# Kernel tuning notes

Hardware: AMD Instinct MI355X
Metric: run time of the kernel (lower is better)

Reference implementation:

```python
import jax, jax.numpy as jnp
import numpy as np

B, S, D, H, DF, L, V, MAXLEN = 8, 1024, 768, 12, 3072, 6, 32000, 2048
HD = D // H
EPS = 1e-5

def _pe(max_length, d_model):
    position = jnp.arange(max_length, dtype=jnp.float32)[:, None]
    i = jnp.arange(d_model, dtype=jnp.float32)[None, :]
    angles = position * (1.0 / jnp.power(10000.0, 2.0 * jnp.floor(i / 2.0) / d_model))
    pe = jnp.zeros((max_length, d_model), dtype=jnp.float32)
    pe = pe.at[:, 0::2].set(jnp.sin(angles[:, 0::2]))
    pe = pe.at[:, 1::2].set(jnp.cos(angles[:, 1::2]))
    return pe

def _layernorm(x, g, b):
    mu = jnp.mean(x, axis=-1, keepdims=True)
    var = jnp.mean((x - mu) ** 2, axis=-1, keepdims=True)
    return (x - mu) * jax.lax.rsqrt(var + EPS) * g + b

def setup_inputs() -> dict:
    key = jax.random.key(0)
    ks = jax.random.split(key, 16)
    s = 0.02
    emb = jax.random.normal(ks[0], (V, D), jnp.float32) * s
    emb = emb.at[0].set(0.0)  # padding_idx=0
    inp = {
        'input_ids': jax.random.randint(ks[1], (B, S), 0, V),
        'emb': emb,
        'pe': _pe(MAXLEN, D),
        'Wq': jax.random.normal(ks[2], (L, D, D), jnp.float32) * s,
        'bq': jnp.zeros((L, D), jnp.float32),
        'Wk': jax.random.normal(ks[3], (L, D, D), jnp.float32) * s,
        'bk': jnp.zeros((L, D), jnp.float32),
        'Wv': jax.random.normal(ks[4], (L, D, D), jnp.float32) * s,
        'bv': jnp.zeros((L, D), jnp.float32),
        'W1': jax.random.normal(ks[5], (L, DF, D), jnp.float32) * s,
        'b1': jnp.zeros((L, DF), jnp.float32),
        'W2': jax.random.normal(ks[6], (L, D, DF), jnp.float32) * s,
        'b2': jnp.zeros((L, D), jnp.float32),
        'ln1_g': jnp.ones((L, D), jnp.float32),
        'ln1_b': jnp.zeros((L, D), jnp.float32),
        'ln2_g': jnp.ones((L, D), jnp.float32),
        'ln2_b': jnp.zeros((L, D), jnp.float32),
    }
    return inp

def _mha(x, Wq, bq, Wk, bk, Wv, bv):
    b, s, _ = x.shape
    q = (x @ Wq.T + bq).reshape(b, H, s, HD)  # faithful to torch .view (no transpose)
    k = (x @ Wk.T + bk).reshape(b, H, s, HD)
    v = (x @ Wv.T + bv).reshape(b, H, s, HD)
    scores = jnp.einsum('bhqd,bhkd->bhqk', q, k) / (HD ** 0.5)
    att = jax.nn.softmax(scores, axis=-1)
    o = jnp.einsum('bhqk,bhkd->bhqd', att, v)
    return o.transpose(0, 2, 1, 3).reshape(b, s, D)

def reference(input_ids, emb, pe, Wq, bq, Wk, bk, Wv, bv, W1, b1, W2, b2, ln1_g, ln1_b, ln2_g, ln2_b):
    x = emb[input_ids] + pe[:input_ids.shape[1], :]
    # dropout is identity in eval mode
    for l in range(L):
        h1 = _mha(x, Wq[l], bq[l], Wk[l], bk[l], Wv[l], bv[l])
        y1 = _layernorm(x + h1, ln1_g[l], ln1_b[l])
        h2 = jax.nn.relu(y1 @ W1[l].T + b1[l]) @ W2[l].T + b2[l]
        x = _layernorm(y1 + h2, ln2_g[l], ln2_b[l])
    return x
```

## Files before the change

kernel.cpp:

```cpp
#include <hip/hip_runtime.h>


typedef _Float16 f16;
typedef _Float16 half4 __attribute__((ext_vector_type(4)));
typedef _Float16 half8 __attribute__((ext_vector_type(8)));
typedef float f32x4 __attribute__((ext_vector_type(4)));
typedef float f32x16 __attribute__((ext_vector_type(16)));

constexpr int Bn = 8, Sn = 1024, Dn = 768, Hn = 12, HDn = 64, DFn = 3072, Ln = 6;
constexpr int BS = Bn * Sn;

__device__ __forceinline__ void glds16(const f16* g, f16* l) {
  __builtin_amdgcn_global_load_lds(
      (const __attribute__((address_space(1))) unsigned int*)g,
      (__attribute__((address_space(3))) unsigned int*)l, 16, 0, 0);
}

__device__ __forceinline__ float ex2(float x) {
#if __has_builtin(__builtin_amdgcn_exp2f)
  return __builtin_amdgcn_exp2f(x);
#else
  return exp2f(x);
#endif
}

__global__ __launch_bounds__(256) void pack_qkv(
    const float* __restrict__ Wq, const float* __restrict__ Wk, const float* __restrict__ Wv,
    const float* __restrict__ bq, const float* __restrict__ bk, const float* __restrict__ bv,
    f16* __restrict__ Wo, float* __restrict__ bo) {
  const long per = (long)Dn * Dn;
  const long t = (long)blockIdx.x * 256 + threadIdx.x;
  const long totalW4 = (long)Ln * 3 * per / 4;
  if (t < totalW4) {
    const long i = t * 4;
    const int l = (int)(i / (3 * per));
    long rem = i - (long)l * 3 * per;
    const int which = (int)(rem / per);
    const long e = rem - (long)which * per;
    const float* s = (which == 0) ? Wq : ((which == 1) ? Wk : Wv);
    const float4 v = *(const float4*)&s[(long)l * per + e];
    half4 h = {(f16)v.x, (f16)v.y, (f16)v.z, (f16)v.w};
    *(half4*)&Wo[i] = h;
  }
  if (t < (long)Ln * 3 * Dn) {
    int l = (int)(t / (3 * Dn));
    int rem = (int)(t % (3 * Dn));
    int which = rem / Dn, c = rem % Dn;
    const float* s = (which == 0) ? bq : ((which == 1) ? bk : bv);
    bo[t] = s[l * Dn + c];
  }
}

__global__ __launch_bounds__(256) void f32_to_f16_k(
    const float* __restrict__ src, f16* __restrict__ dst, long n) {
  long i = ((long)blockIdx.x * 256 + threadIdx.x) * 4;
  if (i < n) {
    float4 v = *(const float4*)&src[i];
    half4 h = {(f16)v.x, (f16)v.y, (f16)v.z, (f16)v.w};
    *(half4*)&dst[i] = h;
  }
}

__global__ __launch_bounds__(256) void embed_k(
    const int* __restrict__ ids, const float* __restrict__ emb, const float* __restrict__ pe,
    float* __restrict__ Xf, f16* __restrict__ Xh) {
  const int row = blockIdx.x;
  const int s = row & (Sn - 1);
  const int id = ids[row];
  const size_t eb = (size_t)id * Dn, pb = (size_t)s * Dn, ob = (size_t)row * Dn;
  for (int c = threadIdx.x; c < Dn; c += 256) {
    float v = emb[eb + c] + pe[pb + c];
    Xf[ob + c] = v;
    Xh[ob + c] = (f16)v;
  }
}

template <int MODE>
__global__ __launch_bounds__(256) void gemm_bt(
    const f16* __restrict__ A, const f16* __restrict__ Bw, const float* __restrict__ bias,
    float* __restrict__ outF, f16* __restrict__ o0, f16* __restrict__ o1, f16* __restrict__ o2,
    int M, int N, int K, int lda) {
  const int m0 = blockIdx.x * 128;
  const int n0 = blockIdx.y * 128;
  const int tid = threadIdx.x;
  const int lane = tid & 63, wave = tid >> 6;
  const int wm = wave & 1, wn = wave >> 1;
  const int l15 = lane & 15, l4 = lane >> 4;

  __shared__ __align__(16) f16 As[128 * 32];
  __shared__ __align__(16) f16 Bs[128 * 32];

  const f32x4 z4 = {0.f, 0.f, 0.f, 0.f};
  f32x4 acc[4][4];
#pragma unroll
  for (int i = 0; i < 4; i++)
#pragma unroll
    for (int j = 0; j < 4; j++) acc[i][j] = z4;

  const int sRow = wave * 32 + (lane >> 2);
  const int sCol = (lane & 3) * 8;
  const int kz = (MODE == 4) ? ((int)blockIdx.z * K) : 0;
  const f16* gA = A + (size_t)(m0 + sRow) * lda + kz + sCol;
  const f16* gB = Bw + (size_t)(n0 + sRow) * lda + kz + sCol;
  f16* lA0 = &As[(wave * 32) * 32];
  f16* lA1 = &As[(wave * 32 + 16) * 32];
  f16* lB0 = &Bs[(wave * 32) * 32];
  f16* lB1 = &Bs[(wave * 32 + 16) * 32];
  const size_t rowStep = (size_t)16 * lda;

  const int kr = 8 * l4;
  for (int k0 = 0; k0 < K; k0 += 32) {
    glds16(gA + k0, lA0);
    glds16(gA + k0 + rowStep, lA1);
    glds16(gB + k0, lB0);
    glds16(gB + k0 + rowStep, lB1);
    __syncthreads();
    half8 af[4], bfr[4];
#pragma unroll
    for (int i = 0; i < 4; i++) af[i] = *(const half8*)&As[(wm * 64 + i * 16 + l15) * 32 + kr];
#pragma unroll
    for (int j = 0; j < 4; j++) bfr[j] = *(const half8*)&Bs[(wn * 64 + j * 16 + l15) * 32 + kr];
#pragma unroll
    for (int i = 0; i < 4; i++)
#pragma unroll
      for (int j = 0; j < 4; j++)
        acc[i][j] = __builtin_amdgcn_mfma_f32_16x16x32_f16(af[i], bfr[j], acc[i][j], 0, 0, 0);
    __syncthreads();
  }

  const int colb = n0 + wn * 64;
  const int rowb = m0 + wm * 64;
#pragma unroll
  for (int j = 0; j < 4; j++) {
    const int col = colb + j * 16 + l15;
    const float bb = (MODE == 4) ? 0.f : bias[col];
#pragma unroll
    for (int i = 0; i < 4; i++) {
      const int rb = rowb + i * 16 + l4 * 4;
#pragma unroll
      for (int r = 0; r < 4; r++) {
        float v = acc[i][j][r] + bb;
        const int row = rb + r;
        if (MODE == 1) {
          v = fmaxf(v, 0.f);
          o0[(size_t)row * N + col] = (f16)v;
        } else if (MODE == 3) {
          const int sel = col / 768;
          const int cl = col - sel * 768;
          f16* op = (sel == 0) ? o0 : ((sel == 1) ? o1 : o2);
          op[(size_t)row * 768 + cl] = (f16)v;
        } else if (MODE == 4) {
          outF[((size_t)blockIdx.z * M + row) * N + col] = v;
        } else {
          o0[(size_t)row * N + col] = (f16)v;
        }
      }
    }
  }
}

__global__ __launch_bounds__(256, 3) void attn_k(
    const f16* __restrict__ Qg, const f16* __restrict__ Kg, const f16* __restrict__ Vg,
    float* __restrict__ O) {
  const int bh = blockIdx.x;
  const int q0 = blockIdx.y * 128;
  const int b = bh / Hn, h = bh - b * Hn;
  const size_t base = (size_t)b * (Sn * Dn) + (size_t)h * (Sn * HDn);
  const f16* Qh = Qg + base;
  const f16* Kh = Kg + base;
  const f16* Vh = Vg + base;

  const int tid = threadIdx.x, lane = tid & 63, wave = tid >> 6;
  const int l31 = lane & 31;
  const int hi = lane >> 5;

  __shared__ __align__(16) f16 Ks[64 * 72];
  __shared__ __align__(16) f16 Vt[64 * 72];

  const int qrow = q0 + wave * 32 + l31;
  half8 qf[4];
#pragma unroll
  for (int m = 0; m < 4; m++)
    qf[m] = *(const half8*)&Qh[(size_t)qrow * HDn + 16 * m + 8 * hi];

  f32x16 Oacc0, Oacc1;
#pragma unroll
  for (int i = 0; i < 16; i++) { Oacc0[i] = 0.f; Oacc1[i] = 0.f; }
  float mrow = -1e30f, lrow = 0.f;
  const float csc = 0.18033688011112042f;

  for (int kt = 0; kt < Sn / 64; ++kt) {
#pragma unroll
    for (int cc = 0; cc < 2; cc++) {
      const int c = tid + cc * 256;
      const int row = c >> 3, col = (c & 7) * 8;
      *(int4*)&Ks[row * 72 + col] = *(const int4*)&Kh[(size_t)(kt * 64 + row) * HDn + col];
    }
#pragma unroll
    for (int ee = 0; ee < 2; ee++) {
      const int e = tid + ee * 256;
      const int hd = e & 63, kpo = e >> 6;
      f16 tmp[8];
#pragma unroll
      for (int j = 0; j < 8; j++)
        tmp[j] = Vh[(size_t)(kt * 64 + kpo * 8 + j) * HDn + hd];
      *(int4*)&Vt[hd * 72 + kpo * 8] = *(const int4*)tmp;
    }
    __syncthreads();

    f32x16 s0, s1;
#pragma unroll
    for (int i = 0; i < 16; i++) { s0[i] = 0.f; s1[i] = 0.f; }
#pragma unroll
    for (int m = 0; m < 4; m++) {
      half8 k0 = *(const half8*)&Ks[l31 * 72 + 16 * m + 8 * hi];
      half8 k1 = *(const half8*)&Ks[(32 + l31) * 72 + 16 * m + 8 * hi];
      s0 = __builtin_amdgcn_mfma_f32_32x32x16_f16(k0, qf[m], s0, 0, 0, 0);
      s1 = __builtin_amdgcn_mfma_f32_32x32x16_f16(k1, qf[m], s1, 0, 0, 0);
    }

    float t8[8];
#pragma unroll
    for (int i = 0; i < 8; i++)
      t8[i] = fmaxf(fmaxf(s0[i], s0[i + 8]), fmaxf(s1[i], s1[i + 8]));
#pragma unroll
    for (int i = 0; i < 4; i++) t8[i] = fmaxf(t8[i], t8[i + 4]);
    float mx = fmaxf(fmaxf(t8[0], t8[1]), fmaxf(t8[2], t8[3]));
    mx = fmaxf(mx, __shfl_xor(mx, 32));
    const float M = fmaxf(mrow, mx * csc);
    const float alpha = ex2(mrow - M);

#pragma unroll
    for (int i = 0; i < 16; i++) {
      s0[i] = ex2(fmaf(s0[i], csc, -M));
      s1[i] = ex2(fmaf(s1[i], csc, -M));
    }
    float r0 = 0.f, r1 = 0.f, r2 = 0.f, r3 = 0.f;
#pragma unroll
    for (int i = 0; i < 16; i += 4) {
      r0 += s0[i]; r1 += s0[i + 1]; r2 += s0[i + 2]; r3 += s0[i + 3];
      r0 += s1[i]; r1 += s1[i + 1]; r2 += s1[i + 2]; r3 += s1[i + 3];
    }
    float rsum = (r0 + r1) + (r2 + r3);
    rsum += __shfl_xor(rsum, 32);
    lrow = lrow * alpha + rsum;
    mrow = M;
#pragma unroll
    for (int i = 0; i < 16; i++) { Oacc0[i] *= alpha; Oacc1[i] *= alpha; }

    unsigned pA[2][4], pB[2][4];
#pragma unroll
    for (int t = 0; t < 4; t++) {
      pA[0][t] = __builtin_bit_cast(unsigned, __builtin_amdgcn_cvt_pkrtz(s0[4 * t + 0], s0[4 * t + 1]));
      pB[0][t] = __builtin_bit_cast(unsigned, __builtin_amdgcn_cvt_pkrtz(s0[4 * t + 2], s0[4 * t + 3]));
      pA[1][t] = __builtin_bit_cast(unsigned, __builtin_amdgcn_cvt_pkrtz(s1[4 * t + 0], s1[4 * t + 1]));
      pB[1][t] = __builtin_bit_cast(unsigned, __builtin_amdgcn_cvt_pkrtz(s1[4 * t + 2], s1[4 * t + 3]));
    }

#pragma unroll
    for (int c = 0; c < 4; c++) {
      const int g = c >> 1, tt = 2 * (c & 1);
      const unsigned ownA = hi ? pA[g][tt + 1] : pA[g][tt];
      const unsigned ownB = hi ? pB[g][tt + 1] : pB[g][tt];
      const unsigned sndA = hi ? pA[g][tt] : pA[g][tt + 1];
      const unsigned sndB = hi ? pB[g][tt] : pB[g][tt + 1];
      const unsigned rA = (unsigned)__shfl_xor((int)sndA, 32);
      const unsigned rB = (unsigned)__shfl_xor((int)sndB, 32);
      int4 w;
      w.x = (int)(hi ? rA : ownA);
      w.y = (int)(hi ? rB : ownB);
      w.z = (int)(hi ? ownA : rA);
      w.w = (int)(hi ? ownB : rB);
      const half8 pf = __builtin_bit_cast(half8, w);
      const half8 v0 = *(const half8*)&Vt[l31 * 72 + 16 * c + 8 * hi];
      const half8 v1 = *(const half8*)&Vt[(32 + l31) * 72 + 16 * c + 8 * hi];
      Oacc0 = __builtin_amdgcn_mfma_f32_32x32x16_f16(v0, pf, Oacc0, 0, 0, 0);
      Oacc1 = __builtin_amdgcn_mfma_f32_32x32x16_f16(v1, pf, Oacc1, 0, 0, 0);
    }
    __syncthreads();
  }

  const float inv = 1.f / lrow;
  float* Orow = O + ((size_t)b * Sn + qrow) * Dn + h * HDn;
#pragma unroll
  for (int t = 0; t < 4; t++) {
    float4 o0, o1;
    o0.x = Oacc0[4 * t + 0] * inv; o0.y = Oacc0[4 * t + 1] * inv;
    o0.z = Oacc0[4 * t + 2] * inv; o0.w = Oacc0[4 * t + 3] * inv;
    o1.x = Oacc1[4 * t + 0] * inv; o1.y = Oacc1[4 * t + 1] * inv;
    o1.z = Oacc1[4 * t + 2] * inv; o1.w = Oacc1[4 * t + 3] * inv;
    *(float4*)&Orow[8 * t + 4 * hi] = o0;
    *(float4*)&Orow[32 + 8 * t + 4 * hi] = o1;
  }
}

__global__ __launch_bounds__(256) void add_ln(
    const float* __restrict__ Xi, const float* __restrict__ Hr,
    const float* __restrict__ g, const float* __restrict__ bt,
    float* __restrict__ Yf, f16* __restrict__ Yh) {
  const int row = blockIdx.x;
  const int tid = threadIdx.x;
  const size_t base = (size_t)row * Dn;
  float v0 = Xi[base + tid] + Hr[base + tid];
  float v1 = Xi[base + tid + 256] + Hr[base + tid + 256];
  float v2 = Xi[base + tid + 512] + Hr[base + tid + 512];

  __shared__ float red[8];
  float s = v0 + v1 + v2;
  for (int off = 32; off; off >>= 1) s += __shfl_down(s, off);
  const int wv = tid >> 6, ln = tid & 63;
  if (ln == 0) red[wv] = s;
  __syncthreads();
  if (tid == 0) red[4] = (red[0] + red[1] + red[2] + red[3]) * (1.f / Dn);
  __syncthreads();
  const float mu = red[4];
  const float d0 = v0 - mu, d1 = v1 - mu, d2 = v2 - mu;
  float vs = d0 * d0 + d1 * d1 + d2 * d2;
  for (int off = 32; off; off >>= 1) vs += __shfl_down(vs, off);
  if (ln == 0) red[wv] = vs;
  __syncthreads();
  if (tid == 0) red[5] = rsqrtf((red[0] + red[1] + red[2] + red[3]) * (1.f / Dn) + 1e-5f);
  __syncthreads();
  const float rs = red[5];
  float y0 = d0 * rs * g[tid] + bt[tid];
  float y1 = d1 * rs * g[tid + 256] + bt[tid + 256];
  float y2 = d2 * rs * g[tid + 512] + bt[tid + 512];
  Yf[base + tid] = y0;        Yh[base + tid] = (f16)y0;
  Yf[base + tid + 256] = y1;  Yh[base + tid + 256] = (f16)y1;
  Yf[base + tid + 512] = y2;  Yh[base + tid + 512] = (f16)y2;
}

__global__ __launch_bounds__(256) void add_ln_sk2(
    const float* __restrict__ Xi, const float* __restrict__ P,
    const float* __restrict__ b2, const float* __restrict__ g, const float* __restrict__ bt,
    float* __restrict__ Yf, f16* __restrict__ Yh) {
  const int row = blockIdx.x;
  const int tid = threadIdx.x;
  const size_t base = (size_t)row * Dn;
  const size_t cs = (size_t)BS * Dn;
  float v0 = Xi[base + tid]       + P[base + tid]       + P[cs + base + tid]       + b2[tid];
  float v1 = Xi[base + tid + 256] + P[base + tid + 256] + P[cs + base + tid + 256] + b2[tid + 256];
  float v2 = Xi[base + tid + 512] + P[base + tid + 512] + P[cs + base + tid + 512] + b2[tid + 512];

  __shared__ float red[8];
  float s = v0 + v1 + v2;
  for (int off = 32; off; off >>= 1) s += __shfl_down(s, off);
  const int wv = tid >> 6, ln = tid & 63;
  if (ln == 0) red[wv] = s;
  __syncthreads();
  if (tid == 0) red[4] = (red[0] + red[1] + red[2] + red[3]) * (1.f / Dn);
  __syncthreads();
  const float mu = red[4];
  const float d0 = v0 - mu, d1 = v1 - mu, d2 = v2 - mu;
  float vs = d0 * d0 + d1 * d1 + d2 * d2;
  for (int off = 32; off; off >>= 1) vs += __shfl_down(vs, off);
  if (ln == 0) red[wv] = vs;
  __syncthreads();
  if (tid == 0) red[5] = rsqrtf((red[0] + red[1] + red[2] + red[3]) * (1.f / Dn) + 1e-5f);
  __syncthreads();
  const float rs = red[5];
  float y0 = d0 * rs * g[tid] + bt[tid];
  float y1 = d1 * rs * g[tid + 256] + bt[tid + 256];
  float y2 = d2 * rs * g[tid + 512] + bt[tid + 512];
  Yf[base + tid] = y0;        Yh[base + tid] = (f16)y0;
  Yf[base + tid + 256] = y1;  Yh[base + tid + 256] = (f16)y1;
  Yf[base + tid + 512] = y2;  Yh[base + tid + 512] = (f16)y2;
}

extern "C" void kernel_launch(void* const* d_in, const int* in_sizes, int n_in,
                              void* d_out, int out_size, void* d_ws, size_t ws_size,
                              hipStream_t stream) {
  const int* ids  = (const int*)d_in[0];
  const float* emb = (const float*)d_in[1];
  const float* pe  = (const float*)d_in[2];
  const float* Wq  = (const float*)d_in[3];
  const float* bq  = (const float*)d_in[4];
  const float* Wk  = (const float*)d_in[5];
  const float* bk  = (const float*)d_in[6];
  const float* Wv  = (const float*)d_in[7];
  const float* bv  = (const float*)d_in[8];
  const float* W1  = (const float*)d_in[9];
  const float* b1  = (const float*)d_in[10];
  const float* W2  = (const float*)d_in[11];
  const float* b2  = (const float*)d_in[12];
  const float* g1  = (const float*)d_in[13];
  const float* be1 = (const float*)d_in[14];
  const float* g2  = (const float*)d_in[15];
  const float* be2 = (const float*)d_in[16];
  float* out = (float*)d_out;

  char* w = (char*)d_ws;
  auto alloc = [&](size_t bytes) {
    char* p = w;
    w += (bytes + 255) & ~(size_t)255;
    return p;
  };
  f16* Wqkv  = (f16*)alloc((size_t)Ln * 3 * Dn * Dn * 2);
  float* bqkv = (float*)alloc((size_t)Ln * 3 * Dn * 4);
  f16* W1h   = (f16*)alloc((size_t)Ln * DFn * Dn * 2);
  f16* W2h   = (f16*)alloc((size_t)Ln * Dn * DFn * 2);
  float* Xf  = (float*)alloc((size_t)BS * Dn * 4);
  f16* Xh    = (f16*)alloc((size_t)BS * Dn * 2);
  f16* Qh    = (f16*)alloc((size_t)BS * Dn * 2);
  f16* Kh    = (f16*)alloc((size_t)BS * Dn * 2);
  f16* Vh    = (f16*)alloc((size_t)BS * Dn * 2);
  float* Of  = (float*)alloc((size_t)BS * Dn * 4);
  float* Y1f = (float*)alloc((size_t)BS * Dn * 4);
  f16* Y1h   = (f16*)alloc((size_t)BS * Dn * 2);
  f16* F1h   = (f16*)alloc((size_t)BS * DFn * 2);

  float* Pf = (float*)Qh;

  {
    const long totalW4 = (long)Ln * 3 * Dn * Dn / 4;
    const int gw = (int)((totalW4 + 255) / 256);
    pack_qkv<<<gw, 256, 0, stream>>>(Wq, Wk, Wv, bq, bk, bv, Wqkv, bqkv);
    const long n1 = (long)Ln * DFn * Dn;
    const int gc = (int)(n1 / 4 / 256);
    f32_to_f16_k<<<gc, 256, 0, stream>>>(W1, W1h, n1);
    f32_to_f16_k<<<gc, 256, 0, stream>>>(W2, W2h, n1);
  }

  embed_k<<<BS, 256, 0, stream>>>(ids, emb, pe, Xf, Xh);

  for (int l = 0; l < Ln; ++l) {
    gemm_bt<3><<<dim3(BS / 128, (3 * Dn) / 128), 256, 0, stream>>>(
        Xh, Wqkv + (size_t)l * 3 * Dn * Dn, bqkv + l * 3 * Dn,
        nullptr, Qh, Kh, Vh, BS, 3 * Dn, Dn, Dn);

    attn_k<<<dim3(Bn * Hn, Sn / 128), 256, 0, stream>>>(Qh, Kh, Vh, Of);

    add_ln<<<BS, 256, 0, stream>>>(Xf, Of, g1 + l * Dn, be1 + l * Dn, Y1f, Y1h);

    gemm_bt<1><<<dim3(BS / 128, DFn / 128), 256, 0, stream>>>(
        Y1h, W1h + (size_t)l * DFn * Dn, b1 + l * DFn,
        nullptr, F1h, nullptr, nullptr, BS, DFn, Dn, Dn);

    gemm_bt<4><<<dim3(BS / 128, Dn / 128, 2), 256, 0, stream>>>(
        F1h, W2h + (size_t)l * Dn * DFn, nullptr,
        Pf, nullptr, nullptr, nullptr, BS, Dn, DFn / 2, DFn);

    float* dstF = (l == Ln - 1) ? out : Xf;
    add_ln_sk2<<<BS, 256, 0, stream>>>(Y1f, Pf, b2 + l * Dn,
                                       g2 + l * Dn, be2 + l * Dn, dstF, Xh);
  }
}
```

Baseline: 1.927 ms.

## Double-buffer LDS tiles in the GEMM to overlap global loads with MFMA

```diff
diff --git a/kernel.cpp b/kernel.cpp
--- a/kernel.cpp
+++ b/kernel.cpp
@@ -87,8 +87,9 @@
   const int wm = wave & 1, wn = wave >> 1;
   const int l15 = lane & 15, l4 = lane >> 4;
 
-  __shared__ __align__(16) f16 As[128 * 32];
-  __shared__ __align__(16) f16 Bs[128 * 32];
+  constexpr int TILE = 128 * 32;
+  __shared__ __align__(16) f16 As[2 * TILE];
+  __shared__ __align__(16) f16 Bs[2 * TILE];
 
   const f32x4 z4 = {0.f, 0.f, 0.f, 0.f};
   f32x4 acc[4][4];
@@ -102,30 +103,38 @@
   const int kz = (MODE == 4) ? ((int)blockIdx.z * K) : 0;
   const f16* gA = A + (size_t)(m0 + sRow) * lda + kz + sCol;
   const f16* gB = Bw + (size_t)(n0 + sRow) * lda + kz + sCol;
-  f16* lA0 = &As[(wave * 32) * 32];
-  f16* lA1 = &As[(wave * 32 + 16) * 32];
-  f16* lB0 = &Bs[(wave * 32) * 32];
-  f16* lB1 = &Bs[(wave * 32 + 16) * 32];
+  f16* lA = &As[(wave * 32) * 32];
+  f16* lB = &Bs[(wave * 32) * 32];
   const size_t rowStep = (size_t)16 * lda;
 
+  auto stage = [&](int buf, int k0) {
+    glds16(gA + k0, lA + buf * TILE);
+    glds16(gA + k0 + rowStep, lA + buf * TILE + 16 * 32);
+    glds16(gB + k0, lB + buf * TILE);
+    glds16(gB + k0 + rowStep, lB + buf * TILE + 16 * 32);
+  };
+
+  stage(0, 0);
+  __syncthreads();
+
   const int kr = 8 * l4;
+  int cur = 0;
   for (int k0 = 0; k0 < K; k0 += 32) {
-    glds16(gA + k0, lA0);
-    glds16(gA + k0 + rowStep, lA1);
-    glds16(gB + k0, lB0);
-    glds16(gB + k0 + rowStep, lB1);
-    __syncthreads();
+    if (k0 + 32 < K) stage(cur ^ 1, k0 + 32);
     half8 af[4], bfr[4];
 #pragma unroll
-    for (int i = 0; i < 4; i++) af[i] = *(const half8*)&As[(wm * 64 + i * 16 + l15) * 32 + kr];
-#pragma unroll
-    for (int j = 0; j < 4; j++) bfr[j] = *(const half8*)&Bs[(wn * 64 + j * 16 + l15) * 32 + kr];
+    for (int i = 0; i < 4; i++)
+      af[i] = *(const half8*)&As[cur * TILE + (wm * 64 + i * 16 + l15) * 32 + kr];
+#pragma unroll
+    for (int j = 0; j < 4; j++)
+      bfr[j] = *(const half8*)&Bs[cur * TILE + (wn * 64 + j * 16 + l15) * 32 + kr];
 #pragma unroll
     for (int i = 0; i < 4; i++)
 #pragma unroll
       for (int j = 0; j < 4; j++)
         acc[i][j] = __builtin_amdgcn_mfma_f32_16x16x32_f16(af[i], bfr[j], acc[i][j], 0, 0, 0);
     __syncthreads();
+    cur ^= 1;
   }
 
   const int colb = n0 + wn * 64;
```

After: 1.816 ms. 5.8% less time.
